# Optimization experiments

Hardware: AMD Instinct MI355X
Metric: run time of the kernel (lower is better)

The kernel has to match this reference:

```python
import jax, jax.numpy as jnp
import numpy as np

NUM_NODES = 16
HSZ = 512
BSZ = 2048


def setup_inputs() -> dict:
    key = jax.random.key(0)
    ks = jax.random.split(key, 5)
    s = 0.02
    return {
        "graphs": jax.random.normal(ks[0], (BSZ, NUM_NODES, HSZ), dtype=jnp.float32),
        "W1": jax.random.normal(ks[1], (NUM_NODES, HSZ, HSZ), dtype=jnp.float32) * s,
        "b1": jnp.zeros((NUM_NODES, HSZ), dtype=jnp.float32),
        "W2": jax.random.normal(ks[2], (NUM_NODES, HSZ, HSZ), dtype=jnp.float32) * s,
        "b2": jnp.zeros((NUM_NODES, HSZ), dtype=jnp.float32),
        "Wg": jax.random.normal(ks[3], (NUM_NODES * HSZ, NUM_NODES), dtype=jnp.float32) * s,
        "bg": jnp.zeros((NUM_NODES,), dtype=jnp.float32),
    }


def reference(graphs, W1, b1, W2, b2, Wg, bg):
    bsz, num_nodes, hsz = graphs.shape
    # Per-node expert MLPs as one batched GEMM over the node axis (fused form
    # of the Python loop over ExpertModel instances).
    h = jax.nn.relu(jnp.einsum('bni,nih->bnh', graphs, W1) + b1)  # (bsz, n, hid)
    outs = jnp.einsum('bnh,nho->bno', h, W2) + b2                 # (bsz, n, out=hsz)
    # torch.cat(outputs, dim=-1).view(bsz, hsz, num_nodes): a raw reshape of the
    # concatenated (bsz, num_nodes*hsz) buffer -- NOT a transpose. Keep it faithful.
    cat = outs.reshape(bsz, num_nodes * hsz).reshape(bsz, hsz, num_nodes)
    # Gating over the flattened graph
    logits = graphs.reshape(bsz, num_nodes * hsz) @ Wg + bg       # (bsz, n)
    expert_probs = jax.nn.softmax(logits, axis=-1)[:, None, :]    # (bsz, 1, n)
    combined = (expert_probs * cat).sum(axis=-1)                  # (bsz, hsz)
    return combined, expert_probs
```

## Files before the change

### kernel.cpp

```cpp
#include <hip/hip_runtime.h>
#include <hip/hip_bf16.h>


typedef __attribute__((ext_vector_type(8))) short bf16x8;
typedef __attribute__((ext_vector_type(4))) float f32x4;

#define OFF_W1T  (0u)
#define OFF_W2T  (8388608u)
#define OFF_H    (16777216u)
#define OFF_PART (50331648u)
#define OFF_PROB (52428800u)

__device__ __forceinline__ void gl2lds16(const void* g, void* l) {
  __builtin_amdgcn_global_load_lds(
      (const __attribute__((address_space(1))) void*)g,
      (__attribute__((address_space(3))) void*)l, 16, 0, 0);
}

__device__ __forceinline__ void cvt16v(const float* __restrict__ src,
                                       bf16x8& lo, bf16x8& hi) {
  float f[16];
  *(float4*)(f + 0)  = *(const float4*)(src + 0);
  *(float4*)(f + 4)  = *(const float4*)(src + 4);
  *(float4*)(f + 8)  = *(const float4*)(src + 8);
  *(float4*)(f + 12) = *(const float4*)(src + 12);
  __hip_bfloat16 t[16];
#pragma unroll
  for (int e = 0; e < 16; e++) t[e] = __float2bfloat16(f[e]);
  lo = *(const bf16x8*)t;
  hi = *(const bf16x8*)(t + 8);
}

__global__ __launch_bounds__(256) void transpose_kernel(
    const float* __restrict__ W1, const float* __restrict__ W2,
    __hip_bfloat16* __restrict__ W1t, __hip_bfloat16* __restrict__ W2t) {
  __shared__ char smem[9216];
  const int bx = blockIdx.x;
  const int ht = bx & 7, kt = bx >> 3;
  const int n = blockIdx.y & 15;
  const float* src = (blockIdx.y >> 4) ? W2 : W1;
  __hip_bfloat16* dst = (blockIdx.y >> 4) ? W2t : W1t;
  src += (size_t)n * 262144;
  dst += (size_t)n * 262144;
  const int tid = threadIdx.x;
  const int hq4 = (tid & 15) * 4, kr = tid >> 4;
#pragma unroll
  for (int rr = 0; rr < 4; rr++) {
    const int kl = rr * 16 + kr;
    float4 v = *(const float4*)(src + (size_t)(kt * 64 + kl) * 512 + ht * 64 + hq4);
    __hip_bfloat16 t4[4] = {__float2bfloat16(v.x), __float2bfloat16(v.y),
                            __float2bfloat16(v.z), __float2bfloat16(v.w)};
#pragma unroll
    for (int i = 0; i < 4; i++)
      *(__hip_bfloat16*)(smem + (hq4 + i) * 144 + kl * 2) = t4[i];
  }
  __syncthreads();
  const int c8 = tid & 7, hr = tid >> 3;
#pragma unroll
  for (int rr = 0; rr < 2; rr++) {
    const int hl = rr * 32 + hr;
    bf16x8 v = *(const bf16x8*)(smem + hl * 144 + c8 * 16);
    *(bf16x8*)(dst + (size_t)(ht * 64 + hl) * 512 + kt * 64 + c8 * 8) = v;
  }
}

__global__ void softmax_kernel(const float* __restrict__ partial,
                               const float* __restrict__ bg,
                               float* __restrict__ probs,
                               float* __restrict__ probs_out) {
  const int r = blockIdx.x * 256 + threadIdx.x;
  float s[16];
#pragma unroll
  for (int j = 0; j < 16; j++) s[j] = 0.f;
  for (int nn = 0; nn < 16; nn++) {
    const float4* p = (const float4*)(partial + ((size_t)nn * 2048 + r) * 16);
#pragma unroll
    for (int c = 0; c < 4; c++) {
      float4 v = p[c];
      s[c * 4 + 0] += v.x; s[c * 4 + 1] += v.y;
      s[c * 4 + 2] += v.z; s[c * 4 + 3] += v.w;
    }
  }
  float mx = -1e30f;
#pragma unroll
  for (int j = 0; j < 16; j++) { s[j] += bg[j]; mx = fmaxf(mx, s[j]); }
  float sum = 0.f;
#pragma unroll
  for (int j = 0; j < 16; j++) { s[j] = __expf(s[j] - mx); sum += s[j]; }
  float inv = 1.f / sum;
#pragma unroll
  for (int j = 0; j < 16; j++) s[j] *= inv;
  float4* pw = (float4*)(probs + (size_t)r * 16);
  float4* ow = (float4*)(probs_out + (size_t)r * 16);
#pragma unroll
  for (int c = 0; c < 4; c++) {
    float4 v = make_float4(s[c*4], s[c*4+1], s[c*4+2], s[c*4+3]);
    pw[c] = v; ow[c] = v;
  }
}

__device__ __forceinline__ void decode_bid(int bid, int& nblk, int& mblk, int& n) {
  int x8 = bid & 7;
  nblk = (bid >> 3) & 3;
  int pair = (bid >> 5) * 8 + x8;
  mblk = pair >> 4;
  n = pair & 15;
}

__global__ __launch_bounds__(256, 4) void gemm1_gate_kernel(
    const float* __restrict__ graphs,
    const __hip_bfloat16* __restrict__ W1t,
    const float* __restrict__ Wg,
    const float* __restrict__ b1,
    __hip_bfloat16* __restrict__ h,
    float* __restrict__ partial) {
  __shared__ char smem[36864];
  const int tid = threadIdx.x, lane = tid & 63, wave = tid >> 6;
  const int q = lane >> 4, l15 = lane & 15;

  if (blockIdx.x >= 1024) {
    const int gbid = blockIdx.x - 1024;
    const int n = gbid & 15, rb = gbid >> 4;
    char* Bt = smem + 8192;
#pragma unroll
    for (int i = 0; i < 2; i++) {
      int k = i * 256 + tid;
      const float* wr_ = Wg + (size_t)(n * 512 + k) * 16;
      float f[16];
      *(float4*)(f + 0)  = *(const float4*)(wr_ + 0);
      *(float4*)(f + 4)  = *(const float4*)(wr_ + 4);
      *(float4*)(f + 8)  = *(const float4*)(wr_ + 8);
      *(float4*)(f + 12) = *(const float4*)(wr_ + 12);
#pragma unroll
      for (int j = 0; j < 16; j++)
        *(__hip_bfloat16*)(Bt + j * 1040 + k * 2) = __float2bfloat16(f[j]);
    }
    __syncthreads();

    const int arow = lane >> 1, ahalf = (lane & 1) * 16;
    const float* Ag = graphs + (size_t)(rb * 32) * 8192 + n * 512 + wave * 128;
    char* Aw = smem + wave * 2048;

    f32x4 acc[2] = {};
    for (int ks = 0; ks < 4; ks++) {
      bf16x8 lo, hi;
      cvt16v(Ag + (size_t)arow * 8192 + ks * 32 + ahalf, lo, hi);
      char* d = Aw + arow * 64 + ahalf * 2;
      *(bf16x8*)d = lo;
      *(bf16x8*)(d + 16) = hi;
      bf16x8 bv = *(const bf16x8*)(Bt + l15 * 1040 + (wave * 128 + ks * 32 + q * 8) * 2);
#pragma unroll
      for (int im = 0; im < 2; im++) {
        bf16x8 av = *(const bf16x8*)(Aw + (im * 16 + l15) * 64 + q * 16);
        acc[im] = __builtin_amdgcn_mfma_f32_16x16x32_bf16(av, bv, acc[im], 0, 0, 0);
      }
    }
#pragma unroll
    for (int im = 0; im < 2; im++)
#pragma unroll
      for (int r = 0; r < 4; r++)
        *(float*)(smem + wave * 2048 + (im * 16 + q * 4 + r) * 64 + l15 * 4) = acc[im][r];
    __syncthreads();
#pragma unroll
    for (int i = 0; i < 2; i++) {
      int c = i * 256 + tid;
      int rrow = c >> 4, j = c & 15;
      float s = 0.f;
#pragma unroll
      for (int w = 0; w < 4; w++) s += *(const float*)(smem + w * 2048 + rrow * 64 + j * 4);
      partial[((size_t)n * 2048 + rb * 32 + rrow) * 16 + j] = s;
    }
    return;
  }

  int nblk, mblk, n;
  decode_bid(blockIdx.x, nblk, mblk, n);
  const int wm = (wave >> 1) * 64, wn = (wave & 1) * 64;
  const int lrow = lane >> 3, lcol = lane & 7;
  const int swz = (lcol ^ lrow) * 8;
  const int xr = l15 & 7;
  const int arow = tid >> 1, ahalf = (tid & 1) * 32;
  const int arx = arow & 7;

  const float* Ag = graphs + (size_t)(mblk * 128) * 8192 + n * 512;
  const __hip_bfloat16* Bg = W1t + (size_t)n * 262144 + (size_t)(nblk * 128) * 512;

  f32x4 acc[4][4] = {};
  for (int ks = 0; ks < 8; ks++) {
    const int k0 = ks * 64;
    const float* asrc = Ag + (size_t)arow * 8192 + k0 + ahalf;
    float f[32];
#pragma unroll
    for (int j = 0; j < 8; j++) *(float4*)(f + j * 4) = *(const float4*)(asrc + j * 4);
#pragma unroll
    for (int i = 0; i < 4; i++) {
      const int r = i * 32 + wave * 8 + lrow;
      gl2lds16(Bg + (size_t)r * 512 + k0 + swz,
               smem + 16384 + i * 4096 + wave * 1024 + lane * 16);
    }
    __hip_bfloat16 t[32];
#pragma unroll
    for (int e = 0; e < 32; e++) t[e] = __float2bfloat16(f[e]);
    char* abase = smem + arow * 128;
#pragma unroll
    for (int j = 0; j < 4; j++) {
      int c = (ahalf >> 3) + j;
      *(bf16x8*)(abase + ((c ^ arx) * 16)) = *(const bf16x8*)(t + j * 8);
    }
    __syncthreads();
#pragma unroll
    for (int hh = 0; hh < 2; hh++) {
      const int co = ((q + hh * 4) ^ xr) * 16;
      bf16x8 av[4], bv[4];
#pragma unroll
      for (int im = 0; im < 4; im++)
        av[im] = *(const bf16x8*)(smem + (wm + im * 16 + l15) * 128 + co);
#pragma unroll
      for (int in = 0; in < 4; in++)
        bv[in] = *(const bf16x8*)(smem + 16384 + (wn + in * 16 + l15) * 128 + co);
#pragma unroll
      for (int im = 0; im < 4; im++)
#pragma unroll
        for (int in = 0; in < 4; in++)
          acc[im][in] = __builtin_amdgcn_mfma_f32_16x16x32_bf16(av[im], bv[in], acc[im][in], 0, 0, 0);
    }
    __syncthreads();
  }

  float bias[4];
#pragma unroll
  for (int in = 0; in < 4; in++)
    bias[in] = b1[n * 512 + nblk * 128 + wn + in * 16 + l15];
  char* epi = smem + wave * 9216;
#pragma unroll
  for (int im = 0; im < 4; im++)
#pragma unroll
    for (int in = 0; in < 4; in++)
#pragma unroll
      for (int r = 0; r < 4; r++) {
        float v = acc[im][in][r] + bias[in];
        v = fmaxf(v, 0.f);
        int rl = im * 16 + q * 4 + r;
        int cl = in * 16 + l15;
        *(__hip_bfloat16*)(epi + rl * 144 + cl * 2) = __float2bfloat16(v);
      }
  __syncthreads();
  __hip_bfloat16* Hg = h + (size_t)(mblk * 128 + wm) * 8192 + n * 512 + nblk * 128 + wn;
#pragma unroll
  for (int it = 0; it < 8; it++) {
    int rl = it * 8 + (lane >> 3);
    int cl = (lane & 7) * 8;
    bf16x8 v = *(const bf16x8*)(epi + rl * 144 + cl * 2);
    *(bf16x8*)(Hg + (size_t)rl * 8192 + cl) = v;
  }
}

__global__ __launch_bounds__(256, 4) void gemm2_kernel(
    const __hip_bfloat16* __restrict__ hbuf,
    const __hip_bfloat16* __restrict__ W2t,
    const float* __restrict__ b2,
    const float* __restrict__ probs,
    float* __restrict__ out) {
  __shared__ char smem[32768];
  const int tid = threadIdx.x, lane = tid & 63, wave = tid >> 6;
  int nblk, mblk, n;
  decode_bid(blockIdx.x, nblk, mblk, n);
  const int wm = (wave >> 1) * 64, wn = (wave & 1) * 64;
  const int q = lane >> 4, l15 = lane & 15;
  const int lrow = lane >> 3, lcol = lane & 7;
  const int swz = (lcol ^ lrow) * 8;
  const int xr = l15 & 7;

  const __hip_bfloat16* Ag = hbuf + (size_t)(mblk * 128) * 8192 + n * 512;
  const __hip_bfloat16* Bg = W2t + (size_t)n * 262144 + (size_t)(nblk * 128) * 512;

  f32x4 acc[4][4] = {};
  for (int ks = 0; ks < 8; ks++) {
    const int k0 = ks * 64;
#pragma unroll
    for (int i = 0; i < 4; i++) {
      const int r = i * 32 + wave * 8 + lrow;
      gl2lds16(Ag + (size_t)r * 8192 + k0 + swz, smem + i * 4096 + wave * 1024 + lane * 16);
      gl2lds16(Bg + (size_t)r * 512 + k0 + swz,
               smem + 16384 + i * 4096 + wave * 1024 + lane * 16);
    }
    __syncthreads();
#pragma unroll
    for (int hh = 0; hh < 2; hh++) {
      const int co = ((q + hh * 4) ^ xr) * 16;
      bf16x8 av[4], bv[4];
#pragma unroll
      for (int im = 0; im < 4; im++)
        av[im] = *(const bf16x8*)(smem + (wm + im * 16 + l15) * 128 + co);
#pragma unroll
      for (int in = 0; in < 4; in++)
        bv[in] = *(const bf16x8*)(smem + 16384 + (wn + in * 16 + l15) * 128 + co);
#pragma unroll
      for (int im = 0; im < 4; im++)
#pragma unroll
        for (int in = 0; in < 4; in++)
          acc[im][in] = __builtin_amdgcn_mfma_f32_16x16x32_bf16(av[im], bv[in], acc[im][in], 0, 0, 0);
    }
    __syncthreads();
  }

  float bias[4];
#pragma unroll
  for (int in = 0; in < 4; in++)
    bias[in] = b2[n * 512 + nblk * 128 + wn + in * 16 + l15];
  float* comb = (float*)smem;
#pragma unroll
  for (int im = 0; im < 4; im++)
#pragma unroll
    for (int r = 0; r < 4; r++) {
      int rl = wm + im * 16 + q * 4 + r;
      float pv = probs[(size_t)(mblk * 128 + rl) * 16 + l15];
#pragma unroll
      for (int in = 0; in < 4; in++) {
        float v = (acc[im][in][r] + bias[in]) * pv;
        v += __shfl_xor(v, 1);
        v += __shfl_xor(v, 2);
        v += __shfl_xor(v, 4);
        v += __shfl_xor(v, 8);
        if (l15 == 0) comb[rl * 8 + (wn >> 4) + in] = v;
      }
    }
  __syncthreads();
  if (tid < 128) {
    float4 v0 = *(const float4*)(comb + tid * 8);
    float4 v1 = *(const float4*)(comb + tid * 8 + 4);
    float* orow = out + (size_t)(mblk * 128 + tid) * 512 + n * 32 + nblk * 8;
    *(float4*)orow = v0;
    *(float4*)(orow + 4) = v1;
  }
}

extern "C" void kernel_launch(void* const* d_in, const int* in_sizes, int n_in,
                              void* d_out, int out_size, void* d_ws, size_t ws_size,
                              hipStream_t stream) {
  const float* graphs = (const float*)d_in[0];
  const float* W1 = (const float*)d_in[1];
  const float* b1 = (const float*)d_in[2];
  const float* W2 = (const float*)d_in[3];
  const float* b2 = (const float*)d_in[4];
  const float* Wg = (const float*)d_in[5];
  const float* bg = (const float*)d_in[6];
  float* out = (float*)d_out;

  char* ws = (char*)d_ws;
  __hip_bfloat16* W1t = (__hip_bfloat16*)(ws + OFF_W1T);
  __hip_bfloat16* W2t = (__hip_bfloat16*)(ws + OFF_W2T);
  __hip_bfloat16* hb  = (__hip_bfloat16*)(ws + OFF_H);
  float* partial = (float*)(ws + OFF_PART);
  float* probs   = (float*)(ws + OFF_PROB);

  transpose_kernel<<<dim3(64, 32), 256, 0, stream>>>(W1, W2, W1t, W2t);
  gemm1_gate_kernel<<<2048, 256, 0, stream>>>(graphs, W1t, Wg, b1, hb, partial);
  softmax_kernel<<<8, 256, 0, stream>>>(partial, bg, probs, out + 2048 * 512);
  gemm2_kernel<<<1024, 256, 0, stream>>>(hb, W2t, b2, probs, out);
}
```

Before: 211.9 us.

## Pre-convert graphs to bf16 with fused gate GEMM, then use async-LDS GEMM1

```diff
diff --git a/kernel.cpp b/kernel.cpp
--- a/kernel.cpp
+++ b/kernel.cpp
@@ -10,6 +10,8 @@
 #define OFF_H    (16777216u)
 #define OFF_PART (50331648u)
 #define OFF_PROB (52428800u)
+#define OFF_GB   (52559872u)
+#define WS_NEED_NEW (86114304ull)
 
 __device__ __forceinline__ void gl2lds16(const void* g, void* l) {
   __builtin_amdgcn_global_load_lds(
@@ -105,6 +107,173 @@
   int pair = (bid >> 5) * 8 + x8;
   mblk = pair >> 4;
   n = pair & 15;
+}
+
+__global__ __launch_bounds__(256, 3) void convert_gate_kernel(
+    const float* __restrict__ graphs,
+    const float* __restrict__ Wg,
+    __hip_bfloat16* __restrict__ gb,
+    float* __restrict__ partial) {
+  __shared__ char smem[49664];
+  const int tid = threadIdx.x, lane = tid & 63, wave = tid >> 6;
+  const int q = lane >> 4, l15 = lane & 15;
+  const int n = blockIdx.x & 15, rb = blockIdx.x >> 4;
+  char* Bt = smem + 33024;
+  char* Aw = smem + wave * 8256;
+
+  const int arow = lane >> 1, ahalf = (lane & 1) * 16;
+  const float* Ag = graphs + (size_t)(rb * 32) * 8192 + n * 512 + wave * 128;
+
+  float g[2][16];
+  {
+    const float* ap = Ag + (size_t)arow * 8192 + ahalf;
+#pragma unroll
+    for (int j = 0; j < 4; j++) *(float4*)(g[0] + j * 4) = *(const float4*)(ap + j * 4);
+  }
+
+#pragma unroll
+  for (int i = 0; i < 2; i++) {
+    int k = i * 256 + tid;
+    const float* wr_ = Wg + (size_t)(n * 512 + k) * 16;
+    float f[16];
+    *(float4*)(f + 0)  = *(const float4*)(wr_ + 0);
+    *(float4*)(f + 4)  = *(const float4*)(wr_ + 4);
+    *(float4*)(f + 8)  = *(const float4*)(wr_ + 8);
+    *(float4*)(f + 12) = *(const float4*)(wr_ + 12);
+#pragma unroll
+    for (int j = 0; j < 16; j++)
+      *(__hip_bfloat16*)(Bt + j * 1040 + k * 2) = __float2bfloat16(f[j]);
+  }
+  __syncthreads();
+
+  f32x4 acc[2] = {};
+#pragma unroll
+  for (int ks = 0; ks < 4; ks++) {
+    if (ks < 3) {
+      const float* ap = Ag + (size_t)arow * 8192 + (ks + 1) * 32 + ahalf;
+#pragma unroll
+      for (int j = 0; j < 4; j++)
+        *(float4*)(g[(ks + 1) & 1] + j * 4) = *(const float4*)(ap + j * 4);
+    }
+    const float* gc = g[ks & 1];
+    __hip_bfloat16 t[16];
+#pragma unroll
+    for (int e = 0; e < 16; e++) t[e] = __float2bfloat16(gc[e]);
+    bf16x8 lo = *(const bf16x8*)t, hi = *(const bf16x8*)(t + 8);
+    char* d = Aw + arow * 256 + (ks * 32 + ahalf) * 2;
+    *(bf16x8*)d = lo;
+    *(bf16x8*)(d + 16) = hi;
+    bf16x8 bv = *(const bf16x8*)(Bt + l15 * 1040 + (wave * 128 + ks * 32 + q * 8) * 2);
+#pragma unroll
+    for (int im = 0; im < 2; im++) {
+      bf16x8 av = *(const bf16x8*)(Aw + (im * 16 + l15) * 256 + ks * 64 + q * 16);
+      acc[im] = __builtin_amdgcn_mfma_f32_16x16x32_bf16(av, bv, acc[im], 0, 0, 0);
+    }
+  }
+  __syncthreads();
+
+#pragma unroll
+  for (int im = 0; im < 2; im++)
+#pragma unroll
+    for (int r = 0; r < 4; r++)
+      *(float*)(smem + 33024 + wave * 2048 + (im * 16 + q * 4 + r) * 64 + l15 * 4) = acc[im][r];
+
+  __hip_bfloat16* gbase = gb + (size_t)(rb * 32) * 8192 + n * 512;
+#pragma unroll
+  for (int r = 0; r < 8; r++) {
+    int u = r * 256 + tid;
+    int row = u >> 6, cu = u & 63;
+    bf16x8 v = *(const bf16x8*)(smem + (cu >> 4) * 8256 + row * 256 + (cu & 15) * 16);
+    *(bf16x8*)(gbase + (size_t)row * 8192 + cu * 8) = v;
+  }
+  __syncthreads();
+
+#pragma unroll
+  for (int i = 0; i < 2; i++) {
+    int c = i * 256 + tid;
+    int rrow = c >> 4, j = c & 15;
+    float s = 0.f;
+#pragma unroll
+    for (int w = 0; w < 4; w++)
+      s += *(const float*)(smem + 33024 + w * 2048 + rrow * 64 + j * 4);
+    partial[((size_t)n * 2048 + rb * 32 + rrow) * 16 + j] = s;
+  }
+}
+
+__global__ __launch_bounds__(256, 4) void gemm1_kernel(
+    const __hip_bfloat16* __restrict__ gbuf,
+    const __hip_bfloat16* __restrict__ W1t,
+    const float* __restrict__ b1,
+    __hip_bfloat16* __restrict__ h) {
+  __shared__ char smem[36864];
+  const int tid = threadIdx.x, lane = tid & 63, wave = tid >> 6;
+  int nblk, mblk, n;
+  decode_bid(blockIdx.x, nblk, mblk, n);
+  const int wm = (wave >> 1) * 64, wn = (wave & 1) * 64;
+  const int q = lane >> 4, l15 = lane & 15;
+  const int lrow = lane >> 3, lcol = lane & 7;
+  const int swz = (lcol ^ lrow) * 8;
+  const int xr = l15 & 7;
+
+  const __hip_bfloat16* Ag = gbuf + (size_t)(mblk * 128) * 8192 + n * 512;
+  const __hip_bfloat16* Bg = W1t + (size_t)n * 262144 + (size_t)(nblk * 128) * 512;
+
+  f32x4 acc[4][4] = {};
+  for (int ks = 0; ks < 8; ks++) {
+    const int k0 = ks * 64;
+#pragma unroll
+    for (int i = 0; i < 4; i++) {
+      const int r = i * 32 + wave * 8 + lrow;
+      gl2lds16(Ag + (size_t)r * 8192 + k0 + swz, smem + i * 4096 + wave * 1024 + lane * 16);
+      gl2lds16(Bg + (size_t)r * 512 + k0 + swz,
+               smem + 16384 + i * 4096 + wave * 1024 + lane * 16);
+    }
+    __syncthreads();
+#pragma unroll
+    for (int hh = 0; hh < 2; hh++) {
+      const int co = ((q + hh * 4) ^ xr) * 16;
+      bf16x8 av[4], bv[4];
+#pragma unroll
+      for (int im = 0; im < 4; im++)
+        av[im] = *(const bf16x8*)(smem + (wm + im * 16 + l15) * 128 + co);
+#pragma unroll
+      for (int in = 0; in < 4; in++)
+        bv[in] = *(const bf16x8*)(smem + 16384 + (wn + in * 16 + l15) * 128 + co);
+#pragma unroll
+      for (int im = 0; im < 4; im++)
+#pragma unroll
+        for (int in = 0; in < 4; in++)
+          acc[im][in] = __builtin_amdgcn_mfma_f32_16x16x32_bf16(av[im], bv[in], acc[im][in], 0, 0, 0);
+    }
+    __syncthreads();
+  }
+
+  float bias[4];
+#pragma unroll
+  for (int in = 0; in < 4; in++)
+    bias[in] = b1[n * 512 + nblk * 128 + wn + in * 16 + l15];
+  char* epi = smem + wave * 9216;
+#pragma unroll
+  for (int im = 0; im < 4; im++)
+#pragma unroll
+    for (int in = 0; in < 4; in++)
+#pragma unroll
+      for (int r = 0; r < 4; r++) {
+        float v = acc[im][in][r] + bias[in];
+        v = fmaxf(v, 0.f);
+        int rl = im * 16 + q * 4 + r;
+        int cl = in * 16 + l15;
+        *(__hip_bfloat16*)(epi + rl * 144 + cl * 2) = __float2bfloat16(v);
+      }
+  __syncthreads();
+  __hip_bfloat16* Hg = h + (size_t)(mblk * 128 + wm) * 8192 + n * 512 + nblk * 128 + wn;
+#pragma unroll
+  for (int it = 0; it < 8; it++) {
+    int rl = it * 8 + (lane >> 3);
+    int cl = (lane & 7) * 8;
+    bf16x8 v = *(const bf16x8*)(epi + rl * 144 + cl * 2);
+    *(bf16x8*)(Hg + (size_t)rl * 8192 + cl) = v;
+  }
 }
 
 __global__ __launch_bounds__(256, 4) void gemm1_gate_kernel(
@@ -355,7 +524,15 @@
   float* probs   = (float*)(ws + OFF_PROB);
 
   transpose_kernel<<<dim3(64, 32), 256, 0, stream>>>(W1, W2, W1t, W2t);
-  gemm1_gate_kernel<<<2048, 256, 0, stream>>>(graphs, W1t, Wg, b1, hb, partial);
-  softmax_kernel<<<8, 256, 0, stream>>>(partial, bg, probs, out + 2048 * 512);
+
+  if (ws_size >= WS_NEED_NEW) {
+    __hip_bfloat16* gbb = (__hip_bfloat16*)(ws + OFF_GB);
+    convert_gate_kernel<<<1024, 256, 0, stream>>>(graphs, Wg, gbb, partial);
+    softmax_kernel<<<8, 256, 0, stream>>>(partial, bg, probs, out + 2048 * 512);
+    gemm1_kernel<<<1024, 256, 0, stream>>>(gbb, W1t, b1, hb);
+  } else {
+    gemm1_gate_kernel<<<2048, 256, 0, stream>>>(graphs, W1t, Wg, b1, hb, partial);
+    softmax_kernel<<<8, 256, 0, stream>>>(partial, bg, probs, out + 2048 * 512);
+  }
   gemm2_kernel<<<1024, 256, 0, stream>>>(hb, W2t, b2, probs, out);
 }
```

Result: faster. 202.7 us (-4.3%).
